# Optimization experiments

Hardware: AMD Instinct MI355X
Metric: run time of the kernel (lower is better)

## Reference

```python
import jax, jax.numpy as jnp
import numpy as np

B, S, D = 4, 2048, 2048
H, Dh, Dl = 16, 128, 128  # head_dim must equal latent_dim for the source matmul to type-check


def setup_inputs() -> dict:
    key = jax.random.key(0)
    ks = jax.random.split(key, 6)
    sc = 0.02
    return {
        "hidden_states": jax.random.normal(ks[0], (B, S, D), dtype=jnp.float32),
        "Wq": jax.random.normal(ks[1], (H * Dh, D), dtype=jnp.float32) * sc,
        "Wk_down": jax.random.normal(ks[2], (H * Dl, D), dtype=jnp.float32) * sc,
        "Wv_down": jax.random.normal(ks[3], (H * Dl, D), dtype=jnp.float32) * sc,
        "Wk_up": jax.random.normal(ks[4], (H * Dh, H * Dl), dtype=jnp.float32) * sc,
        "Wo": jax.random.normal(ks[5], (D, H * Dh), dtype=jnp.float32) * sc,
    }


def reference(hidden_states, Wq, Wk_down, Wv_down, Wk_up, Wo):
    # projections (torch Linear: y = x @ W.T)
    q = (hidden_states @ Wq.T).reshape(B, S, H, Dh).transpose(0, 2, 1, 3)        # [B,H,S,Dh]
    k_lat = (hidden_states @ Wk_down.T).reshape(B, S, H, Dl).transpose(0, 2, 1, 3)  # [B,H,S,Dl]
    v_lat = (hidden_states @ Wv_down.T).reshape(B, S, H, Dl).transpose(0, 2, 1, 3)  # [B,H,S,Dl]

    scores = jnp.einsum("bhsd,bhtd->bhst", q, k_lat) / jnp.sqrt(jnp.float32(Dl))
    attn = jax.nn.softmax(scores, axis=-1)
    out_lat = jnp.einsum("bhst,bhtd->bhsd", attn, v_lat)                          # [B,H,S,Dl]
    out_lat = out_lat.transpose(0, 2, 1, 3).reshape(B, S, H * Dl)

    # source bug (faithful): k_up_proj is applied to the attention output
    up = out_lat @ Wk_up.T                                                         # [B,S,H*Dh]
    return up @ Wo.T                                                               # [B,S,D]
```

## Files before the change

kernel.cpp:

```cpp
#include <hip/hip_runtime.h>
#include <hip/hip_bf16.h>
#include <stdint.h>

typedef unsigned short u16;
typedef __attribute__((ext_vector_type(4))) float f32x4;
typedef __attribute__((ext_vector_type(8))) short s16x8;
typedef __attribute__((ext_vector_type(4))) u16 u16x4;

__device__ __forceinline__ u16 f2bf(float x) {
  union { float f; uint32_t u; } v; v.f = x;
  uint32_t r = v.u + 0x7FFFu + ((v.u >> 16) & 1u);
  return (u16)(r >> 16);
}
__device__ __forceinline__ u16 f2bfh(float x) {
  __hip_bfloat16 h = __float2bfloat16(x);
  u16 r; __builtin_memcpy(&r, &h, 2); return r;
}

__device__ __forceinline__ void gload16(const void* g, const void* l) {
  __builtin_amdgcn_global_load_lds((const __attribute__((address_space(1))) void*)g,
                                   (__attribute__((address_space(3))) void*)l,
                                   16, 0, 0);
}

__global__ void fill_k(float* out, int n, float v) {
  for (int i = blockIdx.x * blockDim.x + threadIdx.x; i < n; i += gridDim.x * blockDim.x)
    out[i] = v;
}

__global__ void cvtall_k(const float* __restrict__ hs, const float* __restrict__ Wq,
                         const float* __restrict__ Wkd, const float* __restrict__ Wvd,
                         const float* __restrict__ Wo,
                         u16* __restrict__ hsB, u16* __restrict__ W3, u16* __restrict__ WoB) {
  int i = blockIdx.x * blockDim.x + threadIdx.x;
  const float* src; u16* dst; int off;
  if (i < 4194304)      { src = hs;  dst = hsB;          off = i; }
  else if (i < 5242880) { src = Wq;  dst = W3;           off = i - 4194304; }
  else if (i < 6291456) { src = Wkd; dst = W3 + 4194304; off = i - 5242880; }
  else if (i < 7340032) { src = Wvd; dst = W3 + 8388608; off = i - 6291456; }
  else                  { src = Wo;  dst = WoB;          off = i - 7340032; }
  f32x4 v = ((const f32x4*)src)[off];
  u16x4 o;
  o.x = f2bf(v.x); o.y = f2bf(v.y); o.z = f2bf(v.z); o.w = f2bf(v.w);
  ((u16x4*)dst)[off] = o;
}

__global__ void cvtT_k(const float* __restrict__ in, u16* __restrict__ out) {
  __shared__ float t[32][33];
  int tx = threadIdx.x, ty = threadIdx.y;
  int c = blockIdx.x * 32 + tx;
#pragma unroll
  for (int j = 0; j < 4; ++j) {
    int r = blockIdx.y * 32 + ty + j * 8;
    t[ty + j * 8][tx] = in[(size_t)r * 2048 + c];
  }
  __syncthreads();
  int c2 = blockIdx.y * 32 + tx;
#pragma unroll
  for (int j = 0; j < 4; ++j) {
    int r2 = blockIdx.x * 32 + ty + j * 8;
    out[(size_t)r2 * 2048 + c2] = f2bf(t[tx][ty + j * 8]);
  }
}

template <typename CT, int OUTMODE, bool VOUT>
__global__ __launch_bounds__(256) void btgemm_k(const u16* __restrict__ A0,
                                                const u16* __restrict__ B0,
                                                CT* __restrict__ C,
                                                u16* __restrict__ Vt,
                                                int M, int N, int K) {
  __shared__ u16 As[128 * 64];
  __shared__ u16 Bs[128 * 64];
  int nnt = N >> 7;
  int bid = blockIdx.x;
  int nwg = gridDim.x;
  if ((nwg & 7) == 0) { int q = nwg >> 3; bid = (bid & 7) * q + (bid >> 3); }
  int mt = bid / nnt, nt = bid - mt * nnt;
  int tid = threadIdx.x, wave = tid >> 6, lane = tid & 63;
  int l15 = lane & 15, l4 = lane >> 4;
  int wr = wave >> 1, wc = wave & 1;
  int sr = lane >> 3, sc = lane & 7;
  int gsl = (sc ^ sr) * 8;

  const u16* Ag = A0 + (size_t)(mt * 128 + wave * 32 + sr) * K + gsl;
  const u16* Bg = B0 + (size_t)(nt * 128 + wave * 32 + sr) * K + gsl;
  u16* Asw = As + wave * 32 * 64;
  u16* Bsw = Bs + wave * 32 * 64;

  f32x4 acc[4][4];
#pragma unroll
  for (int i = 0; i < 4; ++i)
#pragma unroll
    for (int j = 0; j < 4; ++j) acc[i][j] = f32x4{0.f, 0.f, 0.f, 0.f};

  for (int kt = 0; kt < K; kt += 64) {
#pragma unroll
    for (int i = 0; i < 4; ++i) {
      gload16(Ag + kt + i * 8 * K, Asw + i * 512);
      gload16(Bg + kt + i * 8 * K, Bsw + i * 512);
    }
    __syncthreads();
#pragma unroll
    for (int kk = 0; kk < 2; ++kk) {
      s16x8 af[4], bfr[4];
#pragma unroll
      for (int mf = 0; mf < 4; ++mf) {
        int row = wr * 64 + mf * 16 + l15;
        int sl = ((kk * 4 + l4) ^ (row & 7)) * 8;
        af[mf] = *(const s16x8*)(As + row * 64 + sl);
      }
#pragma unroll
      for (int nf = 0; nf < 4; ++nf) {
        int row = wc * 64 + nf * 16 + l15;
        int sl = ((kk * 4 + l4) ^ (row & 7)) * 8;
        bfr[nf] = *(const s16x8*)(Bs + row * 64 + sl);
      }
#pragma unroll
      for (int mf = 0; mf < 4; ++mf)
#pragma unroll
        for (int nf = 0; nf < 4; ++nf)
          acc[mf][nf] = __builtin_amdgcn_mfma_f32_16x16x32_bf16(af[mf], bfr[nf], acc[mf][nf], 0, 0, 0);
    }
    __syncthreads();
  }

  int crow = mt * 128 + wr * 64 + l4 * 4;
  int ccol = nt * 128 + wc * 64 + l15;
#pragma unroll
  for (int mf = 0; mf < 4; ++mf)
#pragma unroll
    for (int nf = 0; nf < 4; ++nf) {
      int col = ccol + nf * 16;
      int row0 = crow + mf * 16;
      if (VOUT && col >= 4096) {
        int h = (col - 4096) >> 7, dh = (col - 4096) & 127;
        int b = row0 >> 11, s0 = row0 & 2047;
        u16x4 w;
        w.x = f2bfh(acc[mf][nf][0]); w.y = f2bfh(acc[mf][nf][1]);
        w.z = f2bfh(acc[mf][nf][2]); w.w = f2bfh(acc[mf][nf][3]);
        *(u16x4*)(Vt + ((size_t)((b << 4) + h) * 128 + dh) * 2048 + s0) = w;
      } else {
#pragma unroll
        for (int r = 0; r < 4; ++r) {
          size_t idx = (size_t)(row0 + r) * N + col;
          float v = acc[mf][nf][r];
          if constexpr (OUTMODE == 0) C[idx] = v; else C[idx] = f2bfh(v);
        }
      }
    }
}

__global__ __launch_bounds__(512, 4) void attn8_k(const u16* __restrict__ qkv,
                                                  const u16* __restrict__ Vt,
                                                  u16* __restrict__ outl) {
  __shared__ u16 Ks[64 * 128];
  __shared__ u16 Vs[128 * 64];
  __shared__ u16 Ps2[8 * 16 * 64];

  int bid = blockIdx.x;
  int xcd = bid & 7, slot = bid >> 3;
  int bh = xcd * 8 + (slot >> 4), qb = slot & 15;
  int b = bh >> 4, h = bh & 15;
  int tid = threadIdx.x, wave = tid >> 6, lane = tid & 63;
  int l15 = lane & 15, l4 = lane >> 4;
  int q0 = qb * 128 + wave * 16;
  const float ksc = 0.12751743f;

  s16x8 qf[4];
#pragma unroll
  for (int kf = 0; kf < 4; ++kf)
    qf[kf] = *(const s16x8*)(qkv + (size_t)(b * 2048 + q0 + l15) * 6144 +
                             h * 128 + kf * 32 + l4 * 8);

  f32x4 po[8];
  float smrun = -1e30f, lrun = 0.f;
#pragma unroll
  for (int n2 = 0; n2 < 8; ++n2) po[n2] = f32x4{0.f, 0.f, 0.f, 0.f};

  char* PsW = (char*)Ps2 + wave * 2048;

  int krow_b = wave * 8;
  int vrow_b = wave * 16;
  int kj = lane & 15;
  int vj = lane & 7;

  s16x8 kr[2], vr[2];
#define GLOAD_TILE(kv0)                                                                  \
  _Pragma("unroll") for (int i = 0; i < 2; ++i) {                                        \
    int row = krow_b + i * 4 + (lane >> 4);                                              \
    kr[i] = *(const s16x8*)(qkv + (size_t)(b * 2048 + (kv0) + row) * 6144 + 2048 +       \
                            h * 128 + kj * 8);                                           \
    int row2 = vrow_b + i * 8 + (lane >> 3);                                             \
    vr[i] = *(const s16x8*)(Vt + (size_t)(bh * 128 + row2) * 2048 + (kv0) + vj * 8);     \
  }

  GLOAD_TILE(0)

  for (int t = 0; t < 32; ++t) {
    __syncthreads();
#pragma unroll
    for (int i = 0; i < 2; ++i) {
      int row = krow_b + i * 4 + (lane >> 4);
      *(s16x8*)(Ks + row * 128 + ((kj ^ (row & 7)) * 8)) = kr[i];
      int row2 = vrow_b + i * 8 + (lane >> 3);
      *(s16x8*)(Vs + row2 * 64 + ((vj ^ (row2 & 7)) * 8)) = vr[i];
    }
    __syncthreads();
    if (t < 31) GLOAD_TILE((t + 1) * 64)

    f32x4 sa[4];
#pragma unroll
    for (int nf = 0; nf < 4; ++nf) sa[nf] = f32x4{0.f, 0.f, 0.f, 0.f};
    __builtin_amdgcn_s_setprio(1);
#pragma unroll
    for (int kf = 0; kf < 4; ++kf) {
      s16x8 kb[4];
#pragma unroll
      for (int nf = 0; nf < 4; ++nf) {
        int row = nf * 16 + l15;
        int sl = ((kf * 4 + l4) ^ (row & 7)) * 8;
        kb[nf] = *(const s16x8*)(Ks + row * 128 + sl);
      }
#pragma unroll
      for (int nf = 0; nf < 4; ++nf)
        sa[nf] = __builtin_amdgcn_mfma_f32_16x16x32_bf16(kb[nf], qf[kf], sa[nf], 0, 0, 0);
    }
    __builtin_amdgcn_s_setprio(0);

    {
      float m01 = fmaxf(fmaxf(sa[0][0], sa[0][1]), fmaxf(sa[0][2], sa[0][3]));
      float m23 = fmaxf(fmaxf(sa[1][0], sa[1][1]), fmaxf(sa[1][2], sa[1][3]));
      float m45 = fmaxf(fmaxf(sa[2][0], sa[2][1]), fmaxf(sa[2][2], sa[2][3]));
      float m67 = fmaxf(fmaxf(sa[3][0], sa[3][1]), fmaxf(sa[3][2], sa[3][3]));
      float pmax = fmaxf(fmaxf(m01, m23), fmaxf(m45, m67));
      pmax = fmaxf(pmax, __shfl_xor(pmax, 16, 64));
      pmax = fmaxf(pmax, __shfl_xor(pmax, 32, 64));
      float smax = pmax * ksc;
      if (!__all(smax - smrun <= 8.0f)) {
        float mnew = fmaxf(smrun, smax);
        float fsc = exp2f(smrun - mnew);
        lrun *= fsc;
#pragma unroll
        for (int n2 = 0; n2 < 8; ++n2)
#pragma unroll
          for (int r = 0; r < 4; ++r) po[n2][r] *= fsc;
        smrun = mnew;
      }
      int row = l15;
      int swz = (row & 7) << 4;
      float ssum = 0.f;
#pragma unroll
      for (int nf = 0; nf < 4; ++nf) {
        float p0 = exp2f(fmaf(sa[nf][0], ksc, -smrun));
        float p1 = exp2f(fmaf(sa[nf][1], ksc, -smrun));
        float p2 = exp2f(fmaf(sa[nf][2], ksc, -smrun));
        float p3 = exp2f(fmaf(sa[nf][3], ksc, -smrun));
        ssum += (p0 + p1) + (p2 + p3);
        u16x4 w;
        w.x = f2bfh(p0); w.y = f2bfh(p1); w.z = f2bfh(p2); w.w = f2bfh(p3);
        *(u16x4*)(PsW + row * 128 + (((nf * 4 + l4) * 8) ^ swz)) = w;
      }
      ssum += __shfl_xor(ssum, 16, 64);
      ssum += __shfl_xor(ssum, 32, 64);
      lrun += ssum;
    }

    s16x8 pb[2];
    {
      int row = l15;
      int swz = (row & 7) << 4;
#pragma unroll
      for (int k2 = 0; k2 < 2; ++k2)
        pb[k2] = *(const s16x8*)(PsW + row * 128 + ((k2 * 64 + l4 * 16) ^ swz));
    }

    __builtin_amdgcn_s_setprio(1);
#pragma unroll
    for (int n2 = 0; n2 < 8; ++n2) {
#pragma unroll
      for (int k2 = 0; k2 < 2; ++k2) {
        int row = n2 * 16 + l15;
        int sl = ((k2 * 4 + l4) ^ (row & 7)) * 8;
        s16x8 vb = *(const s16x8*)(Vs + row * 64 + sl);
        po[n2] = __builtin_amdgcn_mfma_f32_16x16x32_bf16(vb, pb[k2], po[n2], 0, 0, 0);
      }
    }
    __builtin_amdgcn_s_setprio(0);
  }
#undef GLOAD_TILE

  {
    float inv = 1.0f / lrun;
#pragma unroll
    for (int n2 = 0; n2 < 8; ++n2) {
      u16x4 w;
      w.x = f2bfh(po[n2][0] * inv);
      w.y = f2bfh(po[n2][1] * inv);
      w.z = f2bfh(po[n2][2] * inv);
      w.w = f2bfh(po[n2][3] * inv);
      *(u16x4*)(outl + (size_t)(b * 2048 + q0 + l15) * 2048 + h * 128 + n2 * 16 + l4 * 4) = w;
    }
  }
}

extern "C" void kernel_launch(void* const* d_in, const int* in_sizes, int n_in,
                              void* d_out, int out_size, void* d_ws, size_t ws_size,
                              hipStream_t stream) {
  (void)in_sizes; (void)n_in;
  const float* hs  = (const float*)d_in[0];
  const float* Wq  = (const float*)d_in[1];
  const float* Wkd = (const float*)d_in[2];
  const float* Wvd = (const float*)d_in[3];
  const float* Wku = (const float*)d_in[4];
  const float* Wo  = (const float*)d_in[5];
  float* out = (float*)d_out;
  char* ws = (char*)d_ws;

  if (ws_size < 201326592ull) {
    fill_k<<<4096, 256, 0, stream>>>(out, out_size, 1e9f);
    return;
  }

  u16* W3   = (u16*)(ws);
  u16* WcH  = (u16*)(ws + 25165824);
  u16* hsB  = (u16*)(ws + 33554432);
  u16* outl = (u16*)(ws + 33554432);
  u16* qkv  = (u16*)(ws + 67108864);
  u16* WoB  = (u16*)(ws + 167772160);
  u16* WkuT = (u16*)(ws + 176160768);
  u16* Vt   = (u16*)(ws + 167772160);

  cvtall_k<<<32768, 256, 0, stream>>>(hs, Wq, Wkd, Wvd, Wo, hsB, W3, WoB);
  cvtT_k<<<dim3(64, 64), dim3(32, 8), 0, stream>>>(Wku, WkuT);

  btgemm_k<u16, 1, false><<<256, 256, 0, stream>>>(WoB, WkuT, WcH, nullptr, 2048, 2048, 2048);

  btgemm_k<u16, 1, true><<<3072, 256, 0, stream>>>(hsB, W3, qkv, Vt, 8192, 6144, 2048);

  attn8_k<<<1024, 512, 0, stream>>>(qkv, Vt, outl);

  btgemm_k<float, 0, false><<<1024, 256, 0, stream>>>(outl, WcH, out, nullptr, 8192, 2048, 2048);
}
```

Measured before the change: 591.9 us.

## Merge weight-combine GEMM into QKV GEMM launch and double-buffer attention K/V

Folds the Wo·Wk_up weight-combine GEMM into the QKV projection launch as extra tiles, removing a launch and its tail. The Q/K output buffer drops the unused V columns, shrinking the row stride and write traffic. The attention kernel double-buffers K/V tiles in LDS to remove one barrier per iteration, at the cost of more LDS per block and possibly lower occupancy.

Result: faster. 579.3 us (-2.1%).

```diff
diff --git a/kernel.cpp b/kernel.cpp
--- a/kernel.cpp
+++ b/kernel.cpp
@@ -63,11 +63,100 @@
   }
 }
 
-template <typename CT, int OUTMODE, bool VOUT>
+__global__ __launch_bounds__(256) void gemm_qkvwc_k(const u16* __restrict__ hsB,
+                                                    const u16* __restrict__ W3,
+                                                    u16* __restrict__ qk,
+                                                    u16* __restrict__ Vt,
+                                                    const u16* __restrict__ WoB,
+                                                    const u16* __restrict__ WkuT,
+                                                    u16* __restrict__ WcH) {
+  __shared__ u16 As[128 * 64];
+  __shared__ u16 Bs[128 * 64];
+  int bid = blockIdx.x;
+  int bid2 = (bid & 7) * 416 + (bid >> 3);
+  const u16 *A0, *B0;
+  int mt, nt; bool isW;
+  if (bid2 < 3072) { isW = false; mt = bid2 / 48; nt = bid2 - mt * 48; A0 = hsB; B0 = W3; }
+  else { int ix = bid2 - 3072; isW = true; mt = ix >> 4; nt = ix & 15; A0 = WoB; B0 = WkuT; }
+  const int K = 2048;
+  int tid = threadIdx.x, wave = tid >> 6, lane = tid & 63;
+  int l15 = lane & 15, l4 = lane >> 4;
+  int wr = wave >> 1, wc = wave & 1;
+  int sr = lane >> 3, sc = lane & 7;
+  int gsl = (sc ^ sr) * 8;
+
+  const u16* Ag = A0 + (size_t)(mt * 128 + wave * 32 + sr) * K + gsl;
+  const u16* Bg = B0 + (size_t)(nt * 128 + wave * 32 + sr) * K + gsl;
+  u16* Asw = As + wave * 32 * 64;
+  u16* Bsw = Bs + wave * 32 * 64;
+
+  f32x4 acc[4][4];
+#pragma unroll
+  for (int i = 0; i < 4; ++i)
+#pragma unroll
+    for (int j = 0; j < 4; ++j) acc[i][j] = f32x4{0.f, 0.f, 0.f, 0.f};
+
+  for (int kt = 0; kt < K; kt += 64) {
+#pragma unroll
+    for (int i = 0; i < 4; ++i) {
+      gload16(Ag + kt + i * 8 * K, Asw + i * 512);
+      gload16(Bg + kt + i * 8 * K, Bsw + i * 512);
+    }
+    __syncthreads();
+#pragma unroll
+    for (int kk = 0; kk < 2; ++kk) {
+      s16x8 af[4], bfr[4];
+#pragma unroll
+      for (int mf = 0; mf < 4; ++mf) {
+        int row = wr * 64 + mf * 16 + l15;
+        int sl = ((kk * 4 + l4) ^ (row & 7)) * 8;
+        af[mf] = *(const s16x8*)(As + row * 64 + sl);
+      }
+#pragma unroll
+      for (int nf = 0; nf < 4; ++nf) {
+        int row = wc * 64 + nf * 16 + l15;
+        int sl = ((kk * 4 + l4) ^ (row & 7)) * 8;
+        bfr[nf] = *(const s16x8*)(Bs + row * 64 + sl);
+      }
+#pragma unroll
+      for (int mf = 0; mf < 4; ++mf)
+#pragma unroll
+        for (int nf = 0; nf < 4; ++nf)
+          acc[mf][nf] = __builtin_amdgcn_mfma_f32_16x16x32_bf16(af[mf], bfr[nf], acc[mf][nf], 0, 0, 0);
+    }
+    __syncthreads();
+  }
+
+  int crow = mt * 128 + wr * 64 + l4 * 4;
+  int ccol = nt * 128 + wc * 64 + l15;
+#pragma unroll
+  for (int mf = 0; mf < 4; ++mf)
+#pragma unroll
+    for (int nf = 0; nf < 4; ++nf) {
+      int col = ccol + nf * 16;
+      int row0 = crow + mf * 16;
+      if (isW) {
+#pragma unroll
+        for (int r = 0; r < 4; ++r)
+          WcH[(size_t)(row0 + r) * 2048 + col] = f2bfh(acc[mf][nf][r]);
+      } else if (col >= 4096) {
+        int h = (col - 4096) >> 7, dh = (col - 4096) & 127;
+        int b = row0 >> 11, s0 = row0 & 2047;
+        u16x4 w;
+        w.x = f2bfh(acc[mf][nf][0]); w.y = f2bfh(acc[mf][nf][1]);
+        w.z = f2bfh(acc[mf][nf][2]); w.w = f2bfh(acc[mf][nf][3]);
+        *(u16x4*)(Vt + ((size_t)((b << 4) + h) * 128 + dh) * 2048 + s0) = w;
+      } else {
+#pragma unroll
+        for (int r = 0; r < 4; ++r)
+          qk[(size_t)(row0 + r) * 4096 + col] = f2bfh(acc[mf][nf][r]);
+      }
+    }
+}
+
 __global__ __launch_bounds__(256) void btgemm_k(const u16* __restrict__ A0,
                                                 const u16* __restrict__ B0,
-                                                CT* __restrict__ C,
-                                                u16* __restrict__ Vt,
+                                                float* __restrict__ C,
                                                 int M, int N, int K) {
   __shared__ u16 As[128 * 64];
   __shared__ u16 Bs[128 * 64];
@@ -129,32 +218,17 @@
 #pragma unroll
   for (int mf = 0; mf < 4; ++mf)
 #pragma unroll
-    for (int nf = 0; nf < 4; ++nf) {
-      int col = ccol + nf * 16;
-      int row0 = crow + mf * 16;
-      if (VOUT && col >= 4096) {
-        int h = (col - 4096) >> 7, dh = (col - 4096) & 127;
-        int b = row0 >> 11, s0 = row0 & 2047;
-        u16x4 w;
-        w.x = f2bfh(acc[mf][nf][0]); w.y = f2bfh(acc[mf][nf][1]);
-        w.z = f2bfh(acc[mf][nf][2]); w.w = f2bfh(acc[mf][nf][3]);
-        *(u16x4*)(Vt + ((size_t)((b << 4) + h) * 128 + dh) * 2048 + s0) = w;
-      } else {
-#pragma unroll
-        for (int r = 0; r < 4; ++r) {
-          size_t idx = (size_t)(row0 + r) * N + col;
-          float v = acc[mf][nf][r];
-          if constexpr (OUTMODE == 0) C[idx] = v; else C[idx] = f2bfh(v);
-        }
-      }
-    }
-}
-
-__global__ __launch_bounds__(512, 4) void attn8_k(const u16* __restrict__ qkv,
+    for (int nf = 0; nf < 4; ++nf)
+#pragma unroll
+      for (int r = 0; r < 4; ++r)
+        C[(size_t)(crow + mf * 16 + r) * N + (ccol + nf * 16)] = acc[mf][nf][r];
+}
+
+__global__ __launch_bounds__(512, 4) void attn9_k(const u16* __restrict__ qk,
                                                   const u16* __restrict__ Vt,
                                                   u16* __restrict__ outl) {
-  __shared__ u16 Ks[64 * 128];
-  __shared__ u16 Vs[128 * 64];
+  __shared__ u16 Ks[2][64 * 128];
+  __shared__ u16 Vs[2][128 * 64];
   __shared__ u16 Ps2[8 * 16 * 64];
 
   int bid = blockIdx.x;
@@ -169,7 +243,7 @@
   s16x8 qf[4];
 #pragma unroll
   for (int kf = 0; kf < 4; ++kf)
-    qf[kf] = *(const s16x8*)(qkv + (size_t)(b * 2048 + q0 + l15) * 6144 +
+    qf[kf] = *(const s16x8*)(qk + (size_t)(b * 2048 + q0 + l15) * 4096 +
                              h * 128 + kf * 32 + l4 * 8);
 
   f32x4 po[8];
@@ -188,7 +262,7 @@
 #define GLOAD_TILE(kv0)                                                                  \
   _Pragma("unroll") for (int i = 0; i < 2; ++i) {                                        \
     int row = krow_b + i * 4 + (lane >> 4);                                              \
-    kr[i] = *(const s16x8*)(qkv + (size_t)(b * 2048 + (kv0) + row) * 6144 + 2048 +       \
+    kr[i] = *(const s16x8*)(qk + (size_t)(b * 2048 + (kv0) + row) * 4096 + 2048 +        \
                             h * 128 + kj * 8);                                           \
     int row2 = vrow_b + i * 8 + (lane >> 3);                                             \
     vr[i] = *(const s16x8*)(Vt + (size_t)(bh * 128 + row2) * 2048 + (kv0) + vj * 8);     \
@@ -197,13 +271,15 @@
   GLOAD_TILE(0)
 
   for (int t = 0; t < 32; ++t) {
-    __syncthreads();
+    int cur = t & 1;
+    u16* Ksc = Ks[cur];
+    u16* Vsc = Vs[cur];
 #pragma unroll
     for (int i = 0; i < 2; ++i) {
       int row = krow_b + i * 4 + (lane >> 4);
-      *(s16x8*)(Ks + row * 128 + ((kj ^ (row & 7)) * 8)) = kr[i];
+      *(s16x8*)(Ksc + row * 128 + ((kj ^ (row & 7)) * 8)) = kr[i];
       int row2 = vrow_b + i * 8 + (lane >> 3);
-      *(s16x8*)(Vs + row2 * 64 + ((vj ^ (row2 & 7)) * 8)) = vr[i];
+      *(s16x8*)(Vsc + row2 * 64 + ((vj ^ (row2 & 7)) * 8)) = vr[i];
     }
     __syncthreads();
     if (t < 31) GLOAD_TILE((t + 1) * 64)
@@ -219,7 +295,7 @@
       for (int nf = 0; nf < 4; ++nf) {
         int row = nf * 16 + l15;
         int sl = ((kf * 4 + l4) ^ (row & 7)) * 8;
-        kb[nf] = *(const s16x8*)(Ks + row * 128 + sl);
+        kb[nf] = *(const s16x8*)(Ksc + row * 128 + sl);
       }
 #pragma unroll
       for (int nf = 0; nf < 4; ++nf)
@@ -281,7 +357,7 @@
       for (int k2 = 0; k2 < 2; ++k2) {
         int row = n2 * 16 + l15;
         int sl = ((k2 * 4 + l4) ^ (row & 7)) * 8;
-        s16x8 vb = *(const s16x8*)(Vs + row * 64 + sl);
+        s16x8 vb = *(const s16x8*)(Vsc + row * 64 + sl);
         po[n2] = __builtin_amdgcn_mfma_f32_16x16x32_bf16(vb, pb[k2], po[n2], 0, 0, 0);
       }
     }
@@ -325,19 +401,17 @@
   u16* WcH  = (u16*)(ws + 25165824);
   u16* hsB  = (u16*)(ws + 33554432);
   u16* outl = (u16*)(ws + 33554432);
-  u16* qkv  = (u16*)(ws + 67108864);
-  u16* WoB  = (u16*)(ws + 167772160);
-  u16* WkuT = (u16*)(ws + 176160768);
+  u16* qk   = (u16*)(ws + 67108864);
+  u16* WoB  = (u16*)(ws + 134217728);
+  u16* WkuT = (u16*)(ws + 142606336);
   u16* Vt   = (u16*)(ws + 167772160);
 
   cvtall_k<<<32768, 256, 0, stream>>>(hs, Wq, Wkd, Wvd, Wo, hsB, W3, WoB);
   cvtT_k<<<dim3(64, 64), dim3(32, 8), 0, stream>>>(Wku, WkuT);
 
-  btgemm_k<u16, 1, false><<<256, 256, 0, stream>>>(WoB, WkuT, WcH, nullptr, 2048, 2048, 2048);
-
-  btgemm_k<u16, 1, true><<<3072, 256, 0, stream>>>(hsB, W3, qkv, Vt, 8192, 6144, 2048);
-
-  attn8_k<<<1024, 512, 0, stream>>>(qkv, Vt, outl);
-
-  btgemm_k<float, 0, false><<<1024, 256, 0, stream>>>(outl, WcH, out, nullptr, 8192, 2048, 2048);
-}
+  gemm_qkvwc_k<<<3328, 256, 0, stream>>>(hsB, W3, qk, Vt, WoB, WkuT, WcH);
+
+  attn9_k<<<1024, 512, 0, stream>>>(qk, Vt, outl);
+
+  btgemm_k<<<1024, 256, 0, stream>>>(outl, WcH, out, 8192, 2048, 2048);
+}
```
